# Optimization experiments

Hardware: AMD Instinct MI355X
Metric: run time of the kernel (lower is better)

Reference implementation:

```python
import jax, jax.numpy as jnp
import numpy as np

B, ID, OD = 4096, 2048, 1024


def _conv_softmax(x, w):
    # x: [..., L]; torch Conv1d(1,1,k=3,stride=1,pad=1,bias=False) then softmax(dim=-1)
    L = x.shape[-1]
    xp = jnp.pad(x, [(0, 0)] * (x.ndim - 1) + [(1, 1)])
    y = w[0] * xp[..., 0:L] + w[1] * xp[..., 1:L + 1] + w[2] * xp[..., 2:L + 2]
    return jax.nn.softmax(y, axis=-1)


def _lstm_cell(x, h, c, Wih, Whh, bih, bhh):
    # torch LSTMCell gate order: i, f, g, o
    g = x @ Wih.T + h @ Whh.T + (bih + bhh)
    i, f, gg, o = jnp.split(g, 4, axis=-1)
    c2 = jax.nn.sigmoid(f) * c + jax.nn.sigmoid(i) * jnp.tanh(gg)
    h2 = jax.nn.sigmoid(o) * jnp.tanh(c2)
    return h2, c2


def _lstm_params(key, in_dim, hid):
    k = 1.0 / np.sqrt(hid)
    ks = jax.random.split(key, 4)
    Wih = jax.random.uniform(ks[0], (4 * hid, in_dim), jnp.float32, -k, k)
    Whh = jax.random.uniform(ks[1], (4 * hid, hid), jnp.float32, -k, k)
    bih = jax.random.uniform(ks[2], (4 * hid,), jnp.float32, -k, k)
    bhh = jax.random.uniform(ks[3], (4 * hid,), jnp.float32, -k, k)
    return Wih, Whh, bih, bhh


def setup_inputs() -> dict:
    key = jax.random.key(0)
    ks = jax.random.split(key, 12)
    spec = jax.random.normal(ks[0], (B, ID), jnp.float32)
    Wih1, Whh1, bih1, bhh1 = _lstm_params(ks[1], ID, OD)
    Wih2, Whh2, bih2, bhh2 = _lstm_params(ks[2], ID // 2, OD // 2)
    Wih3, Whh3, bih3, bhh3 = _lstm_params(ks[3], ID // 4, OD // 4)
    Wih4, Whh4, bih4, bhh4 = _lstm_params(ks[4], ID // 8, OD // 8)
    ck = np.sqrt(1.0 / 3.0)  # Conv1d(1,1,3) init bound
    w2_1h = jax.random.uniform(ks[5], (3,), jnp.float32, -ck, ck)
    w2_1c = jax.random.uniform(ks[6], (3,), jnp.float32, -ck, ck)
    w3_2h = jax.random.uniform(ks[7], (3,), jnp.float32, -ck, ck)
    w3_2c = jax.random.uniform(ks[8], (3,), jnp.float32, -ck, ck)
    w4_3h = jax.random.uniform(ks[9], (3,), jnp.float32, -ck, ck)
    w4_3c = jax.random.uniform(ks[10], (3,), jnp.float32, -ck, ck)
    return dict(spec=spec,
                Wih1=Wih1, Whh1=Whh1, bih1=bih1, bhh1=bhh1,
                Wih2=Wih2, Whh2=Whh2, bih2=bih2, bhh2=bhh2,
                Wih3=Wih3, Whh3=Whh3, bih3=bih3, bhh3=bhh3,
                Wih4=Wih4, Whh4=Whh4, bih4=bih4, bhh4=bhh4,
                w2_1h=w2_1h, w2_1c=w2_1c, w3_2h=w3_2h, w3_2c=w3_2c,
                w4_3h=w4_3h, w4_3c=w4_3c)


def reference(spec, Wih1, Whh1, bih1, bhh1, Wih2, Whh2, bih2, bhh2,
              Wih3, Whh3, bih3, bhh3, Wih4, Whh4, bih4, bhh4,
              w2_1h, w2_1c, w3_2h, w3_2c, w4_3h, w4_3c):
    b = spec.shape[0]
    # Level 4: 8 independent steps, fresh zero state each (torch code passes no hidden)
    x4 = spec.reshape(b, 8, ID // 8)
    z4 = jnp.zeros((b, 8, OD // 8), spec.dtype)
    h4, c4 = _lstm_cell(x4, z4, z4, Wih4, Whh4, bih4, bhh4)   # [b,8,OD/8]
    hb4 = _conv_softmax(h4.reshape(b, 4, OD // 4), w4_3h)      # pairs -> [b,4,OD/4]
    cb4 = _conv_softmax(c4.reshape(b, 4, OD // 4), w4_3c)
    # Level 3: 4 independent steps seeded by level-4 blended states
    x3 = spec.reshape(b, 4, ID // 4)
    h3, c3 = _lstm_cell(x3, hb4, cb4, Wih3, Whh3, bih3, bhh3)  # [b,4,OD/4]
    hb3 = _conv_softmax(h3.reshape(b, 2, OD // 2), w3_2h)      # [b,2,OD/2]
    cb3 = _conv_softmax(c3.reshape(b, 2, OD // 2), w3_2c)
    # Level 2: 2 independent steps
    x2 = spec.reshape(b, 2, ID // 2)
    h2, c2 = _lstm_cell(x2, hb3, cb3, Wih2, Whh2, bih2, bhh2)  # [b,2,OD/2]
    hb2 = _conv_softmax(h2.reshape(b, OD), w2_1h)              # [b,OD]
    cb2 = _conv_softmax(c2.reshape(b, OD), w2_1c)
    # Level 1: single full-resolution step; forward returns out1 = h1
    h1, c1 = _lstm_cell(spec, hb2, cb2, Wih1, Whh1, bih1, bhh1)
    return h1
```

## Files before the change

### kernel.cpp

```cpp
#include <hip/hip_runtime.h>


typedef __bf16 bf16x8 __attribute__((ext_vector_type(8)));
typedef float f32x4 __attribute__((ext_vector_type(4)));
typedef unsigned short u16x4 __attribute__((ext_vector_type(4)));

#define AS1 __attribute__((address_space(1)))
#define AS3 __attribute__((address_space(3)))

__device__ __forceinline__ unsigned short f2bf(float f) {
    union { float f; unsigned int i; } v; v.f = f;
    unsigned int r = v.i + 0x7fffu + ((v.i >> 16) & 1u);
    return (unsigned short)(r >> 16);
}
__device__ __forceinline__ float sigm(float x) { return 1.f / (1.f + __expf(-x)); }
__device__ __forceinline__ float tanh_(float x) { float e = __expf(2.f * x); return 1.f - 2.f / (e + 1.f); }

__global__ __launch_bounds__(256) void cvt_spec3(
    const float* __restrict__ spec, unsigned short* __restrict__ sB,
    unsigned short* __restrict__ X, unsigned short* __restrict__ Y, long n4)
{
    const long stride = (long)gridDim.x * blockDim.x;
    for (long i = (long)blockIdx.x * blockDim.x + threadIdx.x; i < n4; i += stride) {
        const float4 v = ((const float4*)spec)[i];
        u16x4 o; o.x = f2bf(v.x); o.y = f2bf(v.y); o.z = f2bf(v.z); o.w = f2bf(v.w);
        ((u16x4*)sB)[i] = o;
        const long b = i >> 9;
        const int c4 = (int)(i & 511);
        *(u16x4*)(X + (b * 4 + (c4 >> 7)) * 768  + ((c4 & 127) << 2)) = o;
        *(u16x4*)(Y + (b * 2 + (c4 >> 8)) * 1536 + ((c4 & 255) << 2)) = o;
    }
}

__global__ __launch_bounds__(256) void cvt_specA(
    const float* __restrict__ spec, unsigned short* __restrict__ dst, long n4)
{
    const long stride = (long)gridDim.x * blockDim.x;
    for (long i = (long)blockIdx.x * blockDim.x + threadIdx.x; i < n4; i += stride) {
        const float4 v = ((const float4*)spec)[i];
        const long m = i >> 9;
        const int col = ((int)(i & 511)) << 2;
        u16x4 o; o.x = f2bf(v.x); o.y = f2bf(v.y); o.z = f2bf(v.z); o.w = f2bf(v.w);
        *(u16x4*)(dst + m * 3072 + col) = o;
    }
}

struct PSeg { const float* src; unsigned short* dst; long g0; int H; int kshift; int dstld; int dstcol; };
struct PArgs { PSeg s[7]; long total; };

__global__ __launch_bounds__(256) void cvt_permW_all(PArgs pa)
{
    const long stride = (long)gridDim.x * blockDim.x;
    for (long gi = (long)blockIdx.x * blockDim.x + threadIdx.x; gi < pa.total; gi += stride) {
        int si = 0;
#pragma unroll
        for (int k = 1; k < 7; ++k) si += (gi >= pa.s[k].g0);
        const PSeg sg = pa.s[si];
        const long i = gi - sg.g0;
        const int kq = 1 << sg.kshift;
        const int p = (int)(i >> sg.kshift);
        const int kk = ((int)i & (kq - 1)) << 2;
        const int o = ((p >> 6) << 4) | (p & 15);
        const int q = (p >> 4) & 3;
        const long r = (long)q * sg.H + o;
        const float4 v = *(const float4*)(sg.src + (r << (sg.kshift + 2)) + kk);
        u16x4 wv; wv.x = f2bf(v.x); wv.y = f2bf(v.y); wv.z = f2bf(v.z); wv.w = f2bf(v.w);
        *(u16x4*)(sg.dst + (long)p * sg.dstld + sg.dstcol + kk) = wv;
    }
}

__global__ __launch_bounds__(256) void bias_all(
    const float* __restrict__ bih1, const float* __restrict__ bhh1,
    const float* __restrict__ bih2, const float* __restrict__ bhh2,
    const float* __restrict__ bih3, const float* __restrict__ bhh3,
    const float* __restrict__ bih4, const float* __restrict__ bhh4,
    float* __restrict__ bs1, float* __restrict__ bs2,
    float* __restrict__ bs3, float* __restrict__ bs4)
{
    const int i = blockIdx.x * 256 + threadIdx.x;
    const float *bih, *bhh; float* dst; int H, j;
    if (i < 4096)      { bih = bih1; bhh = bhh1; dst = bs1; H = 1024; j = i; }
    else if (i < 6144) { bih = bih2; bhh = bhh2; dst = bs2; H = 512;  j = i - 4096; }
    else if (i < 7168) { bih = bih3; bhh = bhh3; dst = bs3; H = 256;  j = i - 6144; }
    else               { bih = bih4; bhh = bhh4; dst = bs4; H = 128;  j = i - 7168; }
    const int o = ((j >> 6) << 4) | (j & 15);
    const int q = (j >> 4) & 3;
    dst[j] = bih[q * H + o] + bhh[q * H + o];
}

#define QUAD(S, NS, BF)                                                                     \
    { _Pragma("unroll") for (int mi = 0; mi < 4; ++mi) {                                    \
        _Pragma("unroll") for (int ni = 0; ni < 2; ++ni) {                                  \
            acc[(S)*4+mi][(NS)*2+ni] = __builtin_amdgcn_mfma_f32_16x16x32_bf16(             \
                aF[mi][0], BF[ni][0], acc[(S)*4+mi][(NS)*2+ni], 0, 0, 0);                   \
            acc[(S)*4+mi][(NS)*2+ni] = __builtin_amdgcn_mfma_f32_16x16x32_bf16(             \
                aF[mi][1], BF[ni][1], acc[(S)*4+mi][(NS)*2+ni], 0, 0, 0);                   \
    } } }

#define GLL(gsrc, loff) __builtin_amdgcn_global_load_lds(                                   \
    (const AS1 void*)(gsrc), (AS3 void*)(lds + (loff)), 16, 0, 0)

#define FENCE asm volatile("" ::: "memory")

template<bool HAS_CIN, bool LAST>
__global__ __launch_bounds__(512, 2) void gemm8(
    const unsigned short* __restrict__ A, const unsigned short* __restrict__ W, const int K,
    const float* __restrict__ bsum, const float* __restrict__ Cin,
    float* __restrict__ Hout, float* __restrict__ Cout, const int H)
{
    __shared__ __align__(16) char lds[131072];
    const int t = threadIdx.x;
    const int w = t >> 6, l = t & 63;
    const int wr = w >> 2, wc = w & 3;

    const int GX = gridDim.x, GY = gridDim.y;
    const int nwg = GX * GY;
    const int bid = (int)blockIdx.y * GX + (int)blockIdx.x;
    const int swz = (bid & 7) * (nwg >> 3) + (bid >> 3);
    const int m0 = (swz / GY) * 256, n0 = (swz % GY) * 256;

    const int colsw = ((l & 7) ^ (l >> 3)) * 8;
    const size_t k128 = (size_t)128 * K;
    const size_t aoff0 = (size_t)(m0 + w * 16 + (l >> 3)) * K + colsw;
    const size_t aoff1 = aoff0 + (size_t)8 * K;
    const size_t boff0 = (size_t)(n0 + w * 16 + (l >> 3)) * K + colsw;
    const size_t boff1 = boff0 + (size_t)8 * K;
    const int sd0 = w * 2048 + l * 16;
    const int sd1 = sd0 + 1024;

    const int lr128 = (l & 15) * 128;
    const int sw0 = (((l >> 4)    ) ^ (l & 7)) * 16;
    const int sw1 = (((l >> 4) + 4) ^ (l & 7)) * 16;

    f32x4 acc[8][4];
#pragma unroll
    for (int i = 0; i < 8; ++i)
#pragma unroll
        for (int j = 0; j < 4; ++j) acc[i][j] = (f32x4){0.f, 0.f, 0.f, 0.f};

    const int NT = K >> 6;

    GLL(A + aoff0, sd0);                      GLL(A + aoff1, sd1);
    GLL(A + aoff0 + k128, 16384 + sd0);       GLL(A + aoff1 + k128, 16384 + sd1);
    GLL(W + boff0, 32768 + sd0);              GLL(W + boff1, 32768 + sd1);
    GLL(W + boff0 + k128, 49152 + sd0);       GLL(W + boff1 + k128, 49152 + sd1);
    GLL(W + boff0 + 64, 98304 + sd0);         GLL(W + boff1 + 64, 98304 + sd1);
    GLL(W + boff0 + k128 + 64, 114688 + sd0); GLL(W + boff1 + k128 + 64, 114688 + sd1);
    GLL(A + aoff0 + 64, 65536 + sd0);         GLL(A + aoff1 + 64, 65536 + sd1);
    asm volatile("s_waitcnt vmcnt(6)" ::: "memory");
    __builtin_amdgcn_s_barrier();
    FENCE;

    bf16x8 aF[4][2], bF0[2][2], bF1[2][2];

    for (int tt = 0; tt < NT; ++tt) {
        const int q = tt & 1, qn = q ^ 1;
        const int rbA = (q << 16) + (wr << 14) + lr128;
        const int rbB = (q << 16) + 32768 + wc * 8192 + lr128;
        const size_t ko1 = (size_t)(tt + 1) * 64;
        const size_t ko2 = (size_t)(tt + 2) * 64;
        const bool st1 = (tt + 1 < NT), st2 = (tt + 2 < NT);

#pragma unroll
        for (int mi = 0; mi < 4; ++mi) {
            aF[mi][0] = *(const bf16x8*)(lds + rbA + mi * 2048 + sw0);
            aF[mi][1] = *(const bf16x8*)(lds + rbA + mi * 2048 + sw1);
        }
#pragma unroll
        for (int ni = 0; ni < 2; ++ni) {
            bF0[ni][0] = *(const bf16x8*)(lds + rbB + ni * 2048 + sw0);
            bF0[ni][1] = *(const bf16x8*)(lds + rbB + ni * 2048 + sw1);
        }
        if (st1) {
            GLL(A + aoff0 + k128 + ko1, (qn << 16) + 16384 + sd0);
            GLL(A + aoff1 + k128 + ko1, (qn << 16) + 16384 + sd1);
        }
        __builtin_amdgcn_s_barrier();
        FENCE;
        __builtin_amdgcn_s_setprio(1);
        QUAD(0, 0, bF0);
        __builtin_amdgcn_s_setprio(0);
        __builtin_amdgcn_s_barrier();
        FENCE;

#pragma unroll
        for (int ni = 0; ni < 2; ++ni) {
            bF1[ni][0] = *(const bf16x8*)(lds + rbB + 4096 + ni * 2048 + sw0);
            bF1[ni][1] = *(const bf16x8*)(lds + rbB + 4096 + ni * 2048 + sw1);
        }
        if (st2) {
            GLL(W + boff0 + ko2, (q << 16) + 32768 + sd0);
            GLL(W + boff1 + ko2, (q << 16) + 32768 + sd1);
        }
        __builtin_amdgcn_s_barrier();
        FENCE;
        __builtin_amdgcn_s_setprio(1);
        QUAD(0, 1, bF1);
        __builtin_amdgcn_s_setprio(0);
        __builtin_amdgcn_s_barrier();
        FENCE;

#pragma unroll
        for (int mi = 0; mi < 4; ++mi) {
            aF[mi][0] = *(const bf16x8*)(lds + rbA + 8192 + mi * 2048 + sw0);
            aF[mi][1] = *(const bf16x8*)(lds + rbA + 8192 + mi * 2048 + sw1);
        }
        if (st2) {
            GLL(W + boff0 + k128 + ko2, (q << 16) + 49152 + sd0);
            GLL(W + boff1 + k128 + ko2, (q << 16) + 49152 + sd1);
        }
        __builtin_amdgcn_s_barrier();
        FENCE;
        __builtin_amdgcn_s_setprio(1);
        QUAD(1, 1, bF1);
        __builtin_amdgcn_s_setprio(0);
        __builtin_amdgcn_s_barrier();
        FENCE;

        if (st2) {
            GLL(A + aoff0 + ko2, (q << 16) + sd0);
            GLL(A + aoff1 + ko2, (q << 16) + sd1);
        }
        if (tt < NT - 2) { asm volatile("s_waitcnt vmcnt(6)" ::: "memory"); }
        else             { asm volatile("s_waitcnt vmcnt(0)" ::: "memory"); }
        __builtin_amdgcn_s_barrier();
        FENCE;
        __builtin_amdgcn_s_setprio(1);
        QUAD(1, 0, bF0);
        __builtin_amdgcn_s_setprio(0);
        __builtin_amdgcn_s_barrier();
        FENCE;
    }

    const int ocol = (n0 >> 6) * 16 + wc * 16 + (l & 15);
    const int bb = n0 + wc * 64 + (l & 15);
    const float b0 = bsum[bb], b1 = bsum[bb + 16], b2 = bsum[bb + 32], b3 = bsum[bb + 48];
    const int mrow0 = m0 + wr * 128 + (l >> 4) * 4;
#pragma unroll
    for (int mi = 0; mi < 8; ++mi)
#pragma unroll
        for (int j = 0; j < 4; ++j) {
            const size_t m = (size_t)(mrow0 + mi * 16 + j);
            const float gi = acc[mi][0][j] + b0;
            const float gf = acc[mi][1][j] + b1;
            const float gg = acc[mi][2][j] + b2;
            const float go = acc[mi][3][j] + b3;
            float c2 = sigm(gi) * tanh_(gg);
            if (HAS_CIN) c2 += sigm(gf) * Cin[m * H + ocol];
            const float h2 = sigm(go) * tanh_(c2);
            Hout[m * H + ocol] = h2;
            if (!LAST) Cout[m * H + ocol] = c2;
        }
}

template<int L>
__global__ __launch_bounds__(256) void conv_dual(
    const float* __restrict__ Hin, const float* __restrict__ Cin,
    const float* __restrict__ w3h, const float* __restrict__ w3c,
    unsigned short* __restrict__ Yb, int ldYb, float* __restrict__ cbuf)
{
    __shared__ float xs[L + 2];
    __shared__ float red[8];
    const int nrows = gridDim.x >> 1;
    const bool isC = (int)blockIdx.x >= nrows;
    const int row = isC ? ((int)blockIdx.x - nrows) : (int)blockIdx.x;
    const float* Xs = isC ? Cin : Hin;
    const float* w3 = isC ? w3c : w3h;
    const int t = threadIdx.x;
    const size_t base = (size_t)row * L;
    const float w0 = w3[0], w1 = w3[1], w2 = w3[2];
    if (t == 0) { xs[0] = 0.f; xs[L + 1] = 0.f; }
    for (int i = t; i < L; i += 256) xs[i + 1] = Xs[base + i];
    __syncthreads();
    constexpr int E = L / 256;
    float y[E];
    float vmax = -3.4e38f;
#pragma unroll
    for (int i = 0; i < E; ++i) {
        const int c = t + i * 256;
        y[i] = w0 * xs[c] + w1 * xs[c + 1] + w2 * xs[c + 2];
        vmax = fmaxf(vmax, y[i]);
    }
#pragma unroll
    for (int off = 32; off >= 1; off >>= 1) vmax = fmaxf(vmax, __shfl_xor(vmax, off));
    if ((t & 63) == 0) red[t >> 6] = vmax;
    __syncthreads();
    vmax = fmaxf(fmaxf(red[0], red[1]), fmaxf(red[2], red[3]));
    float s = 0.f;
#pragma unroll
    for (int i = 0; i < E; ++i) { y[i] = __expf(y[i] - vmax); s += y[i]; }
#pragma unroll
    for (int off = 32; off >= 1; off >>= 1) s += __shfl_xor(s, off);
    if ((t & 63) == 0) red[4 + (t >> 6)] = s;
    __syncthreads();
    const float inv = 1.f / (red[4] + red[5] + red[6] + red[7]);
#pragma unroll
    for (int i = 0; i < E; ++i) {
        const int c = t + i * 256;
        const float v = y[i] * inv;
        if (isC) cbuf[base + c] = v;
        else     Yb[(size_t)row * ldYb + c] = f2bf(v);
    }
}

extern "C" void kernel_launch(void* const* d_in, const int* in_sizes, int n_in,
                              void* d_out, int out_size, void* d_ws, size_t ws_size,
                              hipStream_t stream)
{
    (void)in_sizes; (void)n_in; (void)out_size; (void)ws_size;
    const float* spec  = (const float*)d_in[0];
    const float* Wih1  = (const float*)d_in[1];
    const float* Whh1  = (const float*)d_in[2];
    const float* bih1  = (const float*)d_in[3];
    const float* bhh1  = (const float*)d_in[4];
    const float* Wih2  = (const float*)d_in[5];
    const float* Whh2  = (const float*)d_in[6];
    const float* bih2  = (const float*)d_in[7];
    const float* bhh2  = (const float*)d_in[8];
    const float* Wih3  = (const float*)d_in[9];
    const float* Whh3  = (const float*)d_in[10];
    const float* bih3  = (const float*)d_in[11];
    const float* bhh3  = (const float*)d_in[12];
    const float* Wih4  = (const float*)d_in[13];
    const float* bih4  = (const float*)d_in[15];
    const float* bhh4  = (const float*)d_in[16];
    const float* w2_1h = (const float*)d_in[17];
    const float* w2_1c = (const float*)d_in[18];
    const float* w3_2h = (const float*)d_in[19];
    const float* w3_2c = (const float*)d_in[20];
    const float* w4_3h = (const float*)d_in[21];
    const float* w4_3c = (const float*)d_in[22];

    char* ws = (char*)d_ws;
    float*          h   = (float*)(ws + 0);
    float*          c   = (float*)(ws + (size_t)16777216);
    float*          cb  = (float*)(ws + (size_t)33554432);
    unsigned short* sB  = (unsigned short*)(ws + (size_t)50331648);
    unsigned short* X   = (unsigned short*)(ws + (size_t)67108864);
    unsigned short* Y   = (unsigned short*)(ws + (size_t)92274688);
    unsigned short* Wc1 = (unsigned short*)(ws + (size_t)117440512);
    unsigned short* Wc2 = (unsigned short*)(ws + (size_t)142606336);
    unsigned short* Wc3 = (unsigned short*)(ws + (size_t)148897792);
    unsigned short* W4  = (unsigned short*)(ws + (size_t)150470656);
    float*          bs1 = (float*)(ws + (size_t)150732800);
    float*          bs2 = bs1 + 4096;
    float*          bs3 = bs2 + 4096;
    float*          bs4 = bs3 + 4096;

    cvt_spec3<<<2048, 256, 0, stream>>>(spec, sB, X, Y, 2097152);
    PArgs pa;
    pa.s[0] = { Wih1, Wc1,       0, 1024, 9, 3072,    0 };
    pa.s[1] = { Whh1, Wc1, 2097152, 1024, 8, 3072, 2048 };
    pa.s[2] = { Wih2, Wc2, 3145728,  512, 8, 1536,    0 };
    pa.s[3] = { Whh2, Wc2, 3670016,  512, 7, 1536, 1024 };
    pa.s[4] = { Wih3, Wc3, 3932160,  256, 7,  768,    0 };
    pa.s[5] = { Whh3, Wc3, 4063232,  256, 6,  768,  512 };
    pa.s[6] = { Wih4, W4,  4128768,  128, 6,  256,    0 };
    pa.total = 4161536;
    cvt_permW_all<<<2048, 256, 0, stream>>>(pa);
    bias_all<<<30, 256, 0, stream>>>(bih1, bhh1, bih2, bhh2, bih3, bhh3, bih4, bhh4,
                                     bs1, bs2, bs3, bs4);

    gemm8<false, false><<<dim3(128, 2), 512, 0, stream>>>(sB, W4, 256, bs4, nullptr, h, c, 128);
    conv_dual<256><<<32768, 256, 0, stream>>>(h, c, w4_3h, w4_3c, X + 512, 768, cb);

    gemm8<true, false><<<dim3(64, 4), 512, 0, stream>>>(X, Wc3, 768, bs3, cb, h, c, 256);
    cvt_specA<<<2048, 256, 0, stream>>>(spec, X, 2097152);
    conv_dual<512><<<16384, 256, 0, stream>>>(h, c, w3_2h, w3_2c, Y + 1024, 1536, cb);

    gemm8<true, false><<<dim3(32, 8), 512, 0, stream>>>(Y, Wc2, 1536, bs2, cb, h, c, 512);
    conv_dual<1024><<<8192, 256, 0, stream>>>(h, c, w2_1h, w2_1c, X + 2048, 3072, cb);

    gemm8<true, true><<<dim3(16, 16), 512, 0, stream>>>(X, Wc1, 3072, bs1, cb, (float*)d_out, nullptr, 1024);
}
```

Measured before the change: 317.3 us.

## Restructure GEMM main loop to two barriers per K-tile with merged prefetch

The main K-loop of the LSTM gate GEMM is reorganised from eight barriers per iteration to two. A-tile loads for the next stage are issued together at the top, B-tile loads for stage+2 after the second barrier, and the waitcnt moves to the loop head. All B fragments are read up front so the MFMA quads run back to back. This cuts barrier stalls and lets more MFMA work stay in flight. The cost is more live registers and a changed LDS buffer-reuse schedule that must remain race-free.

Result: slower. 334.1 us (+5.3%).

```diff
diff --git a/kernel.cpp b/kernel.cpp
--- a/kernel.cpp
+++ b/kernel.cpp
@@ -146,10 +146,6 @@
     GLL(W + boff0 + k128, 49152 + sd0);       GLL(W + boff1 + k128, 49152 + sd1);
     GLL(W + boff0 + 64, 98304 + sd0);         GLL(W + boff1 + 64, 98304 + sd1);
     GLL(W + boff0 + k128 + 64, 114688 + sd0); GLL(W + boff1 + k128 + 64, 114688 + sd1);
-    GLL(A + aoff0 + 64, 65536 + sd0);         GLL(A + aoff1 + 64, 65536 + sd1);
-    asm volatile("s_waitcnt vmcnt(6)" ::: "memory");
-    __builtin_amdgcn_s_barrier();
-    FENCE;
 
     bf16x8 aF[4][2], bF0[2][2], bF1[2][2];
 
@@ -157,9 +153,12 @@
         const int q = tt & 1, qn = q ^ 1;
         const int rbA = (q << 16) + (wr << 14) + lr128;
         const int rbB = (q << 16) + 32768 + wc * 8192 + lr128;
-        const size_t ko1 = (size_t)(tt + 1) * 64;
-        const size_t ko2 = (size_t)(tt + 2) * 64;
         const bool st1 = (tt + 1 < NT), st2 = (tt + 2 < NT);
+
+        if (st1) { asm volatile("s_waitcnt vmcnt(4)" ::: "memory"); }
+        else     { asm volatile("s_waitcnt vmcnt(0)" ::: "memory"); }
+        __builtin_amdgcn_s_barrier();
+        FENCE;
 
 #pragma unroll
         for (int mi = 0; mi < 4; ++mi) {
@@ -170,66 +169,39 @@
         for (int ni = 0; ni < 2; ++ni) {
             bF0[ni][0] = *(const bf16x8*)(lds + rbB + ni * 2048 + sw0);
             bF0[ni][1] = *(const bf16x8*)(lds + rbB + ni * 2048 + sw1);
+            bF1[ni][0] = *(const bf16x8*)(lds + rbB + 4096 + ni * 2048 + sw0);
+            bF1[ni][1] = *(const bf16x8*)(lds + rbB + 4096 + ni * 2048 + sw1);
         }
         if (st1) {
+            const size_t ko1 = (size_t)(tt + 1) * 64;
+            GLL(A + aoff0 + ko1, (qn << 16) + sd0);
+            GLL(A + aoff1 + ko1, (qn << 16) + sd1);
             GLL(A + aoff0 + k128 + ko1, (qn << 16) + 16384 + sd0);
             GLL(A + aoff1 + k128 + ko1, (qn << 16) + 16384 + sd1);
         }
-        __builtin_amdgcn_s_barrier();
-        FENCE;
         __builtin_amdgcn_s_setprio(1);
         QUAD(0, 0, bF0);
-        __builtin_amdgcn_s_setprio(0);
-        __builtin_amdgcn_s_barrier();
-        FENCE;
-
-#pragma unroll
-        for (int ni = 0; ni < 2; ++ni) {
-            bF1[ni][0] = *(const bf16x8*)(lds + rbB + 4096 + ni * 2048 + sw0);
-            bF1[ni][1] = *(const bf16x8*)(lds + rbB + 4096 + ni * 2048 + sw1);
-        }
-        if (st2) {
-            GLL(W + boff0 + ko2, (q << 16) + 32768 + sd0);
-            GLL(W + boff1 + ko2, (q << 16) + 32768 + sd1);
-        }
-        __builtin_amdgcn_s_barrier();
-        FENCE;
-        __builtin_amdgcn_s_setprio(1);
         QUAD(0, 1, bF1);
         __builtin_amdgcn_s_setprio(0);
-        __builtin_amdgcn_s_barrier();
-        FENCE;
-
 #pragma unroll
         for (int mi = 0; mi < 4; ++mi) {
             aF[mi][0] = *(const bf16x8*)(lds + rbA + 8192 + mi * 2048 + sw0);
             aF[mi][1] = *(const bf16x8*)(lds + rbA + 8192 + mi * 2048 + sw1);
         }
+        __builtin_amdgcn_s_barrier();
+        FENCE;
+
         if (st2) {
+            const size_t ko2 = (size_t)(tt + 2) * 64;
+            GLL(W + boff0 + ko2, (q << 16) + 32768 + sd0);
+            GLL(W + boff1 + ko2, (q << 16) + 32768 + sd1);
             GLL(W + boff0 + k128 + ko2, (q << 16) + 49152 + sd0);
             GLL(W + boff1 + k128 + ko2, (q << 16) + 49152 + sd1);
         }
-        __builtin_amdgcn_s_barrier();
-        FENCE;
         __builtin_amdgcn_s_setprio(1);
         QUAD(1, 1, bF1);
-        __builtin_amdgcn_s_setprio(0);
-        __builtin_amdgcn_s_barrier();
-        FENCE;
-
-        if (st2) {
-            GLL(A + aoff0 + ko2, (q << 16) + sd0);
-            GLL(A + aoff1 + ko2, (q << 16) + sd1);
-        }
-        if (tt < NT - 2) { asm volatile("s_waitcnt vmcnt(6)" ::: "memory"); }
-        else             { asm volatile("s_waitcnt vmcnt(0)" ::: "memory"); }
-        __builtin_amdgcn_s_barrier();
-        FENCE;
-        __builtin_amdgcn_s_setprio(1);
         QUAD(1, 0, bF0);
         __builtin_amdgcn_s_setprio(0);
-        __builtin_amdgcn_s_barrier();
-        FENCE;
     }
 
     const int ocol = (n0 >> 6) * 16 + wc * 16 + (l & 15);
```
